# Performance work log

Measured on AMD Instinct MI355X. Metric: run time of the kernel, lower is better.

## Reference

```python
import jax, jax.numpy as jnp
import numpy as np

B, N, I, O, CG, H, E = 32, 256, 16, 16, 64, 64, 4096
SEQ_LEN = 256  # sequence_length init arg (temporal attention scale)


def setup_inputs() -> dict:
    key = jax.random.key(0)
    ks = jax.random.split(key, 24)
    r = lambda i, shape, s: jax.random.normal(ks[i], shape, jnp.float32) * s
    return {
        'data': jax.random.normal(ks[0], (B, I, N), jnp.float32),
        'masks': jax.random.bernoulli(ks[1], 0.8, (B, I, N)),
        'edge_index': jax.random.randint(ks[2], (2, E), 0, N, jnp.int64),
        'gcn_w': r(3, (I, CG), 0.2),
        'gcn_b': jnp.zeros((CG,), jnp.float32),
        'sa_qw': r(4, (CG, CG), 0.1), 'sa_qb': jnp.zeros((CG,), jnp.float32),
        'sa_kw': r(5, (CG, CG), 0.1), 'sa_kb': jnp.zeros((CG,), jnp.float32),
        'gru_wih': r(6, (3 * H, I), 0.1), 'gru_whh': r(7, (3 * H, H), 0.1),
        'gru_bih': jnp.zeros((3 * H,), jnp.float32), 'gru_bhh': jnp.zeros((3 * H,), jnp.float32),
        'ta_qw': r(8, (H, H), 0.1), 'ta_qb': jnp.zeros((H,), jnp.float32),
        'ta_kw': r(9, (H, H), 0.1), 'ta_kb': jnp.zeros((H,), jnp.float32),
        'fc1_w': r(10, (H * N * 2, H * N // 4), 0.005), 'fc1_b': jnp.zeros((H * N // 4,), jnp.float32),
        'fc2_w': r(11, (H * N // 4, O * N), 0.01), 'fc2_b': jnp.zeros((O * N,), jnp.float32),
    }


def _forward(data, masks, edge_index, gcn_w, gcn_b, sa_qw, sa_qb, sa_kw, sa_kb,
             gru_wih, gru_whh, gru_bih, gru_bhh, ta_qw, ta_qb, ta_kw, ta_kb,
             fc1_w, fc1_b, fc2_w, fc2_b):
    data = jnp.where(masks, data, 0.0)            # [B, I, N]
    x = jnp.swapaxes(data, 1, 2)                  # [B, N, I] (per-sample node features)

    loop = jnp.arange(N)
    src = jnp.concatenate([edge_index[0], loop])
    dst = jnp.concatenate([edge_index[1], loop])
    w = jnp.concatenate([jnp.ones((E,), jnp.float32), 2.0 * jnp.ones((N,), jnp.float32)])
    deg = jax.ops.segment_sum(w, dst, num_segments=N)
    dinv = jnp.where(deg > 0, jax.lax.rsqrt(deg), 0.0)
    norm = dinv[src] * w * dinv[dst]              # [E+N]
    xw = x @ gcn_w                                # [B, N, CG]
    msg = xw[:, src, :] * norm[None, :, None]     # gather + scale
    agg = jax.vmap(lambda m: jax.ops.segment_sum(m, dst, num_segments=N))(msg)
    h = jax.nn.relu(agg + gcn_b)                  # [B, N, CG]

    # --- SpatialAttention (per sample, scale 1/sqrt(num_nodes)) ---
    q = h @ sa_qw + sa_qb
    k = h @ sa_kw + sa_kb
    att = jax.nn.softmax(jnp.einsum('bnc,bmc->bnm', q, k) / np.sqrt(N).astype(np.float32), axis=-1)
    ha = jnp.einsum('bnm,bmc->bnc', att, h)

    # torch stacks x.T -> [B, CG, N] then .view(B, -1, CG): a reshape, not a transpose
    se = jnp.swapaxes(h, 1, 2).reshape(B, N, CG)
    sa = jnp.swapaxes(ha, 1, 2).reshape(B, N, CG)
    # dropout is identity in eval mode

    # --- GRU (1 layer, batch_first) over rnn_input = data.view(B, -1, I) ---
    rnn_in = data.reshape(B, N, I)
    def step(hprev, xt):
        gi = xt @ gru_wih.T + gru_bih
        gh = hprev @ gru_whh.T + gru_bhh
        ir, iz, inn = jnp.split(gi, 3, axis=-1)
        hr, hz, hn = jnp.split(gh, 3, axis=-1)
        r = jax.nn.sigmoid(ir + hr)
        z = jax.nn.sigmoid(iz + hz)
        n = jnp.tanh(inn + r * hn)
        hnew = (1.0 - z) * n + z * hprev
        return hnew, hnew
    h0 = jnp.zeros((B, H), jnp.float32)
    _, outs = jax.lax.scan(step, h0, jnp.swapaxes(rnn_in, 0, 1))
    rnn_out = jnp.swapaxes(outs, 0, 1)            # [B, N, H]

    # --- TemporalAttention (scale 1/sqrt(sequence_length)) ---
    qt = rnn_out @ ta_qw + ta_qb
    kt = rnn_out @ ta_kw + ta_kb
    att_t = jax.nn.softmax(jnp.einsum('btc,bsc->bts', qt, kt) / np.sqrt(SEQ_LEN).astype(np.float32), axis=-1)
    rnn_a = jnp.einsum('bts,bsc->btc', att_t, rnn_out)

    # --- fused MLP combine ---
    embed = jnp.concatenate([rnn_out, se], axis=-1).reshape(B, -1)  # [B, 2*H*N]
    inter = embed @ fc1_w + fc1_b
    final = inter @ fc2_w + fc2_b
    final = jnp.swapaxes(final.reshape(B, N, O), 1, 2)              # [B, O, N]
    rnn_a = jnp.swapaxes(rnn_a, 1, 2)                               # [B, H, N]
    return final, sa, rnn_a


def reference(data, masks, edge_index, gcn_w, gcn_b, sa_qw, sa_qb, sa_kw, sa_kb,
              gru_wih, gru_whh, gru_bih, gru_bhh, ta_qw, ta_qb, ta_kw, ta_kb,
              fc1_w, fc1_b, fc2_w, fc2_b):
    return _forward(data, masks, edge_index, gcn_w, gcn_b, sa_qw, sa_qb, sa_kw, sa_kb,
                    gru_wih, gru_whh, gru_bih, gru_bhh, ta_qw, ta_qb, ta_kw, ta_kb,
                    fc1_w, fc1_b, fc2_w, fc2_b)
```

## Files before the change

### kernel.cpp

```cpp
#include <hip/hip_runtime.h>

#define NB 32
#define NN 256
#define NI 16
#define NO 16
#define NC 64
#define NH 64
#define NE 4096
#define FC1_N 4096

__device__ __forceinline__ float sigmoidf_(float x){ return 1.0f/(1.0f+__expf(-x)); }
__device__ __forceinline__ float tanhf_(float x){
  float e = __expf(2.0f*x);
  return 1.0f - 2.0f/(e+1.0f);
}

__device__ __forceinline__ void gload16(const void* g, void* l){
  __builtin_amdgcn_global_load_lds((const __attribute__((address_space(1))) void*)g,
                                   (__attribute__((address_space(3))) void*)l, 16, 0, 0);
}

__global__ void k_detect(const unsigned char* __restrict__ m8, const int* __restrict__ ei, int* flags){
  int t = blockIdx.x*256 + threadIdx.x;
  unsigned a = (unsigned)m8[t*4+1] | (unsigned)m8[t*4+2] | (unsigned)m8[t*4+3];
  if (__any(a != 0) && (threadIdx.x & 63) == 0) atomicOr(&flags[0], 1);
  unsigned b = 0;
  if (t < 4096) b = (unsigned)ei[2*t+1];
  if (__any(b != 0) && (threadIdx.x & 63) == 0) atomicOr(&flags[1], 1);
}

__global__ void k_mask(const float* __restrict__ data, const unsigned char* __restrict__ m8,
                       const int* __restrict__ flags, float* __restrict__ dm){
  int i = blockIdx.x*256 + threadIdx.x;
  int mv = flags[0] ? (int)m8[i] : ((const int*)m8)[i];
  dm[i] = mv ? data[i] : 0.0f;
}

__device__ __forceinline__ int edge_src(const int* ei, const int* flags, int e){
  return flags[1] ? ei[e] : ei[2*e];
}
__device__ __forceinline__ int edge_dst(const int* ei, const int* flags, int e){
  return flags[1] ? ei[NE + e] : ei[2*(NE + e)];
}

__global__ __launch_bounds__(256) void k_graph(const int* __restrict__ ei, const int* __restrict__ flags,
                                               float* wadj){
  int t = threadIdx.x;
  float4 z = {0.f,0.f,0.f,0.f};
  for (int x = t; x < 16384; x += 256) ((float4*)wadj)[x] = z;
  __shared__ float degs[NN];
  __shared__ float dls[NN];
  degs[t] = 0.f;
  __syncthreads();
  for (int e = t; e < NE; e += 256) atomicAdd(&degs[edge_dst(ei, flags, e)], 1.0f);
  __syncthreads();
  float di = rsqrtf(degs[t] + 2.0f);
  dls[t] = di;
  atomicAdd(&wadj[t*NN + t], 2.0f*di*di);
  __syncthreads();
  for (int e = t; e < NE; e += 256){
    int s = edge_src(ei, flags, e), d = edge_dst(ei, flags, e);
    atomicAdd(&wadj[d*NN + s], dls[s]*dls[d]);
  }
}

__global__ void k_xw(const float* __restrict__ dm, const float* __restrict__ gw, float* __restrict__ xw){
  int idx = blockIdx.x*256 + threadIdx.x;
  int c = idx & 63, n = (idx>>6) & 255, b = idx>>14;
  const float* dmb = dm + b*NI*NN;
  float a = 0.f;
  #pragma unroll
  for (int i=0;i<NI;i++) a += dmb[i*NN + n]*gw[i*NC + c];
  xw[idx] = a;
}

__global__ void k_agg(const float* __restrict__ wadj, const float* __restrict__ xw,
                      const float* __restrict__ gb, float* __restrict__ h){
  int idx = blockIdx.x*256 + threadIdx.x;
  int c = idx & 63, n = (idx>>6) & 255, b = idx>>14;
  const float* wr = wadj + n*NN;
  const float* xb = xw + b*NN*NC + c;
  float a = gb[c];
  #pragma unroll 4
  for (int m=0;m<NN;m++) a += wr[m]*xb[m*NC];
  h[idx] = fmaxf(a, 0.0f);
}

__global__ void k_qk2(const float* __restrict__ hb, const float* __restrict__ rnn,
    const float* __restrict__ saqw, const float* __restrict__ saqb,
    const float* __restrict__ sakw, const float* __restrict__ sakb,
    const float* __restrict__ taqw, const float* __restrict__ taqb,
    const float* __restrict__ takw, const float* __restrict__ takb,
    float* __restrict__ qb, float* __restrict__ kb, float* __restrict__ qt, float* __restrict__ kt){
  int bid = blockIdx.x;
  const float *src, *qw, *qbias, *kw, *kbias; float *qo, *ko;
  if (bid < 2048){ src=hb; qw=saqw; qbias=saqb; kw=sakw; kbias=sakb; qo=qb; ko=kb; }
  else { bid -= 2048; src=rnn; qw=taqw; qbias=taqb; kw=takw; kbias=takb; qo=qt; ko=kt; }
  int idx = bid*256 + threadIdx.x;
  int c = idx & 63;
  const float* hr = src + (idx>>6)*NC;
  float aq = qbias[c], ak = kbias[c];
  #pragma unroll 8
  for (int cc=0; cc<NC; cc++){ float hv = hr[cc]; aq += hv*qw[cc*NC + c]; ak += hv*kw[cc*NC + c]; }
  qo[idx] = aq; ko[idx] = ak;
}

__global__ __launch_bounds__(256) void k_attn2(const float* __restrict__ qb, const float* __restrict__ kb,
    const float* __restrict__ hb, const float* __restrict__ qt, const float* __restrict__ kt,
    const float* __restrict__ rnn, float* __restrict__ out_sa, float* __restrict__ out_ra){
  int bidx = blockIdx.x;
  const float *q, *kmat, *v; float* outp;
  if (bidx < 1024){ q=qb; kmat=kb; v=hb; outp=out_sa; }
  else { bidx -= 1024; q=qt; kmat=kt; v=rnn; outp=out_ra; }
  int b = bidx >> 5, n0 = (bidx & 31)*8;
  int t = threadIdx.x;
  const float scale = 0.0625f;
  __shared__ __align__(16) float qs[8][64];
  __shared__ float S[8][256];
  #pragma unroll
  for (int rep=0; rep<2; rep++){
    int j = rep*256 + t; int r = j>>6, c = j&63;
    qs[r][c] = q[((b<<8) + n0 + r)*NC + c];
  }
  __syncthreads();
  float4 kr[16];
  const float4* kp = (const float4*)(kmat + ((b<<8) + t)*NC);
  #pragma unroll
  for (int i=0;i<16;i++) kr[i] = kp[i];
  #pragma unroll
  for (int r=0;r<8;r++){
    const float4* q4 = (const float4*)qs[r];
    float s = 0.f;
    #pragma unroll
    for (int i=0;i<16;i++){ float4 a=q4[i], bb=kr[i]; s += a.x*bb.x + a.y*bb.y + a.z*bb.z + a.w*bb.w; }
    S[r][t] = s*scale;
  }
  __syncthreads();
  {
    int g = t>>5, l = t&31;
    float vals[8];
    #pragma unroll
    for (int k2=0;k2<8;k2++) vals[k2] = S[g][l + (k2<<5)];
    float mx = vals[0];
    #pragma unroll
    for (int k2=1;k2<8;k2++) mx = fmaxf(mx, vals[k2]);
    #pragma unroll
    for (int off=16; off; off>>=1) mx = fmaxf(mx, __shfl_xor(mx, off));
    float sm = 0.f;
    #pragma unroll
    for (int k2=0;k2<8;k2++){ vals[k2] = __expf(vals[k2]-mx); sm += vals[k2]; }
    #pragma unroll
    for (int off=16; off; off>>=1) sm += __shfl_xor(sm, off);
    float rS = 1.0f/sm;
    #pragma unroll
    for (int k2=0;k2<8;k2++) S[g][l + (k2<<5)] = vals[k2]*rS;
  }
  __syncthreads();
  int c = t & 63, rp = t >> 6;
  const float* vp = v + (b<<8)*NC + c;
  float a0 = 0.f, a1 = 0.f;
  #pragma unroll 4
  for (int m=0;m<NN;m++){
    float vv = vp[m*NC];
    a0 += S[rp][m]*vv;
    a1 += S[rp+4][m]*vv;
  }
  outp[(((b<<6)+c)<<8) + n0 + rp]     = a0;
  outp[(((b<<6)+c)<<8) + n0 + rp + 4] = a1;
}

__global__ __launch_bounds__(192) void k_gru(const float* __restrict__ dm,
        const float* __restrict__ wih, const float* __restrict__ bih,
        const float* __restrict__ whh, const float* __restrict__ bhh,
        float* __restrict__ rnn){
  int b = blockIdx.x, j = threadIdx.x;
  __shared__ __align__(16) float dmS[4096];
  __shared__ __align__(16) float hs[64];
  __shared__ float gh[192];
  __shared__ float gin[64];
  float wh[64];
  const float4* wr = (const float4*)(whh + j*NH);
  #pragma unroll
  for (int k4=0;k4<16;k4++){ float4 t4 = wr[k4]; wh[4*k4]=t4.x; wh[4*k4+1]=t4.y; wh[4*k4+2]=t4.z; wh[4*k4+3]=t4.w; }
  float wi[16];
  const float4* wir = (const float4*)(wih + j*NI);
  #pragma unroll
  for (int k4=0;k4<4;k4++){ float4 t4 = wir[k4]; wi[4*k4]=t4.x; wi[4*k4+1]=t4.y; wi[4*k4+2]=t4.z; wi[4*k4+3]=t4.w; }
  float bj = bhh[j], bij = bih[j];
  const float4* dmb4 = (const float4*)(dm + b*4096);
  for (int x = j; x < 1024; x += 192) ((float4*)dmS)[x] = dmb4[x];
  if (j < 64) hs[j] = 0.f;
  __syncthreads();
  for (int t=0;t<NN;t++){
    const float* xt = &dmS[t*16];
    float gival = bij;
    #pragma unroll
    for (int i=0;i<16;i++) gival += wi[i]*xt[i];
    float a0=0.f,a1=0.f,a2=0.f,a3=0.f;
    #pragma unroll
    for (int k4=0;k4<16;k4++){
      float4 hv = *(const float4*)&hs[4*k4];
      a0 += wh[4*k4+0]*hv.x; a1 += wh[4*k4+1]*hv.y; a2 += wh[4*k4+2]*hv.z; a3 += wh[4*k4+3]*hv.w;
    }
    float ghv = a0+a1+a2+a3+bj;
    if (j < 128) gh[j] = ghv + gival;
    else { gh[j] = ghv; gin[j-128] = gival; }
    __syncthreads();
    if (j < 64){
      float r  = sigmoidf_(gh[j]);
      float z  = sigmoidf_(gh[j+64]);
      float nn = tanhf_   (gin[j] + r*gh[j+128]);
      float hn = nn + z*(hs[j]-nn);
      rnn[(b*NN + t)*NH + j] = hn;
      hs[j] = hn;
    }
    __syncthreads();
  }
}

__global__ void k_embedT(const float* __restrict__ rnn, const float* __restrict__ h,
                         float* __restrict__ ET){
  int idx = blockIdx.x*256 + threadIdx.x;
  int bb = idx & 31, rr = idx >> 5;
  int n = rr >> 7, c = rr & 127;
  float v;
  if (c < 64) v = rnn[((bb<<8) + n)*NH + c];
  else { int f = (n<<6) + (c-64); v = h[(bb<<14) + ((f&255)<<6) + (f>>8)]; }
  ET[idx] = v;
}

template<int KC>
__global__ __launch_bounds__(512, 4) void k_fc(const float* __restrict__ W,
        const float* __restrict__ Ein, float* __restrict__ part){
  const int tid = threadIdx.x, lane = tid & 63, wv_ = tid >> 6;
  const int cw = wv_ & 1, bq = wv_ >> 1;
  const int c0 = blockIdx.x*512;
  const long k0 = (long)blockIdx.y*KC;
  __shared__ __align__(16) float wlds[2][8][512];
  __shared__ __align__(16) float elds[2][256];
  float acc[4][8];
  #pragma unroll
  for (int c=0;c<4;c++)
    #pragma unroll
    for (int bb=0;bb<8;bb++) acc[c][bb]=0.f;

  const int NCH = KC/8;
  #define STAGE_FC(ch, bf) { \
    const float* wsrc = W + (k0 + (long)(ch)*8)*FC1_N + c0; \
    gload16(wsrc + (long)wv_*FC1_N + lane*4,       &wlds[bf][wv_][0]); \
    gload16(wsrc + (long)wv_*FC1_N + 256 + lane*4, &wlds[bf][wv_][256]); \
    if (wv_ == 0) gload16(Ein + (k0 + (long)(ch)*8)*32 + lane*4, &elds[bf][0]); \
  }

  STAGE_FC(0, 0)
  int cur = 0;
  for (int ch=0; ch<NCH; ch++){
    __syncthreads();
    if (ch+1 < NCH) STAGE_FC(ch+1, cur^1)
    #pragma unroll
    for (int r=0;r<8;r++){
      float4 wv4 = *(const float4*)&wlds[cur][r][cw*256 + lane*4];
      float4 e0 = *(const float4*)&elds[cur][r*32 + bq*8];
      float4 e1 = *(const float4*)&elds[cur][r*32 + bq*8 + 4];
      float ev[8] = {e0.x,e0.y,e0.z,e0.w,e1.x,e1.y,e1.z,e1.w};
      #pragma unroll
      for (int bb=0;bb<8;bb++){
        acc[0][bb] += wv4.x*ev[bb];
        acc[1][bb] += wv4.y*ev[bb];
        acc[2][bb] += wv4.z*ev[bb];
        acc[3][bb] += wv4.w*ev[bb];
      }
    }
    cur ^= 1;
  }
  float* pp = part + (long)blockIdx.y*131072 + (long)(bq*8)*FC1_N + c0 + cw*256 + lane*4;
  #pragma unroll
  for (int bb=0;bb<8;bb++){
    float4 o; o.x=acc[0][bb]; o.y=acc[1][bb]; o.z=acc[2][bb]; o.w=acc[3][bb];
    *(float4*)(pp + (long)bb*FC1_N) = o;
  }
  #undef STAGE_FC
}

__global__ void k_red1(const float* __restrict__ part, const float* __restrict__ bias,
                       float* __restrict__ ITr){
  int idx = blockIdx.x*256 + threadIdx.x;
  int b = idx >> 12, col = idx & 4095;
  float a = bias[col];
  #pragma unroll 16
  for (int y=0;y<64;y++) a += part[(long)y*131072 + b*FC1_N + col];
  ITr[col*32 + b] = a;
}

__global__ void k_red2(const float* __restrict__ part, const float* __restrict__ bias,
                       float* __restrict__ outp){
  int idx = blockIdx.x*256 + threadIdx.x;
  int b = idx >> 12, col = idx & 4095;
  float a = bias[col];
  #pragma unroll 16
  for (int y=0;y<64;y++) a += part[(long)y*131072 + b*FC1_N + col];
  int n = col >> 4, o = col & 15;
  outp[(b<<12) + (o<<8) + n] = a;
}

extern "C" void kernel_launch(void* const* d_in, const int* in_sizes, int n_in,
                              void* d_out, int out_size, void* d_ws, size_t ws_size,
                              hipStream_t stream) {
  const float* data   = (const float*)d_in[0];
  const unsigned char* masks = (const unsigned char*)d_in[1];
  const int* ei       = (const int*)d_in[2];
  const float* gcn_w  = (const float*)d_in[3];
  const float* gcn_b  = (const float*)d_in[4];
  const float* sa_qw  = (const float*)d_in[5];
  const float* sa_qb  = (const float*)d_in[6];
  const float* sa_kw  = (const float*)d_in[7];
  const float* sa_kb  = (const float*)d_in[8];
  const float* wih    = (const float*)d_in[9];
  const float* whh    = (const float*)d_in[10];
  const float* bih    = (const float*)d_in[11];
  const float* bhh    = (const float*)d_in[12];
  const float* ta_qw  = (const float*)d_in[13];
  const float* ta_qb  = (const float*)d_in[14];
  const float* ta_kw  = (const float*)d_in[15];
  const float* ta_kb  = (const float*)d_in[16];
  const float* fc1_w  = (const float*)d_in[17];
  const float* fc1_b  = (const float*)d_in[18];
  const float* fc2_w  = (const float*)d_in[19];
  const float* fc2_b  = (const float*)d_in[20];

  float* dm    = (float*)d_ws;
  float* wadj  = dm + 131072;
  int*   flags = (int*)(wadj + 65536);
  float* xw    = (float*)(flags + 8);
  float* hb    = xw + 524288;
  float* qb    = hb + 524288;
  float* kb    = qb + 524288;
  float* rnn   = kb + 524288;
  float* qt    = rnn + 524288;
  float* kt    = qt + 524288;
  float* ET    = kt + 524288;
  float* ITr   = ET + 1048576;
  float* part1 = ITr + 131072;
  float* part2 = part1 + 64*131072;

  float* out_final = (float*)d_out;
  float* out_sa = out_final + 131072;
  float* out_ra = out_final + 655360;

  hipMemsetAsync(flags, 0, 32, stream);

  k_detect<<<128,256,0,stream>>>(masks, ei, flags);
  k_mask<<<512,256,0,stream>>>(data, masks, flags, dm);
  k_graph<<<1,256,0,stream>>>(ei, flags, wadj);
  k_xw<<<2048,256,0,stream>>>(dm, gcn_w, xw);
  k_gru<<<32,192,0,stream>>>(dm, wih, bih, whh, bhh, rnn);
  k_agg<<<2048,256,0,stream>>>(wadj, xw, gcn_b, hb);
  k_qk2<<<4096,256,0,stream>>>(hb, rnn, sa_qw, sa_qb, sa_kw, sa_kb,
                               ta_qw, ta_qb, ta_kw, ta_kb, qb, kb, qt, kt);
  k_attn2<<<2048,256,0,stream>>>(qb, kb, hb, qt, kt, rnn, out_sa, out_ra);
  k_embedT<<<4096,256,0,stream>>>(rnn, hb, ET);
  { dim3 g(8,64); k_fc<512><<<g,512,0,stream>>>(fc1_w, ET, part1); }
  k_red1<<<512,256,0,stream>>>(part1, fc1_b, ITr);
  { dim3 g(8,64); k_fc<64><<<g,512,0,stream>>>(fc2_w, ITr, part2); }
  k_red2<<<512,256,0,stream>>>(part2, fc2_b, out_final);
}
```

Baseline: 504.3 us.

## Restructure GRU into single-wavefront blocks and vectorize FC reduction kernels

The GRU kernel drops from 192 to 64 threads per block, so each thread computes all three gate dot products for its hidden unit. This removes one of the two block barriers per timestep and the shared-memory exchange of gate values, but each thread now holds about 3x more weight registers and does 3x the serial FMA work. The two partial-sum reduction kernels now load float4 values with a quarter of the blocks, and the GRU launch moves earlier in the stream. Pressure from the larger register arrays could cause spills.

```diff
diff --git a/kernel.cpp b/kernel.cpp
--- a/kernel.cpp
+++ b/kernel.cpp
@@ -169,51 +169,71 @@
   outp[(((b<<6)+c)<<8) + n0 + rp + 4] = a1;
 }
 
-__global__ __launch_bounds__(192) void k_gru(const float* __restrict__ dm,
+__global__ __launch_bounds__(64) void k_gru(const float* __restrict__ dm,
         const float* __restrict__ wih, const float* __restrict__ bih,
         const float* __restrict__ whh, const float* __restrict__ bhh,
         float* __restrict__ rnn){
-  int b = blockIdx.x, j = threadIdx.x;
+  const int b = blockIdx.x, j = threadIdx.x;
   __shared__ __align__(16) float dmS[4096];
-  __shared__ __align__(16) float hs[64];
-  __shared__ float gh[192];
-  __shared__ float gin[64];
-  float wh[64];
-  const float4* wr = (const float4*)(whh + j*NH);
-  #pragma unroll
-  for (int k4=0;k4<16;k4++){ float4 t4 = wr[k4]; wh[4*k4]=t4.x; wh[4*k4+1]=t4.y; wh[4*k4+2]=t4.z; wh[4*k4+3]=t4.w; }
-  float wi[16];
-  const float4* wir = (const float4*)(wih + j*NI);
-  #pragma unroll
-  for (int k4=0;k4<4;k4++){ float4 t4 = wir[k4]; wi[4*k4]=t4.x; wi[4*k4+1]=t4.y; wi[4*k4+2]=t4.z; wi[4*k4+3]=t4.w; }
-  float bj = bhh[j], bij = bih[j];
+  __shared__ __align__(16) float hsS[64];
   const float4* dmb4 = (const float4*)(dm + b*4096);
-  for (int x = j; x < 1024; x += 192) ((float4*)dmS)[x] = dmb4[x];
-  if (j < 64) hs[j] = 0.f;
-  __syncthreads();
+  float4* dmS4 = (float4*)dmS;
+  #pragma unroll
+  for (int x=0;x<16;x++) dmS4[j + 64*x] = dmb4[j + 64*x];
+  float wr_[64], wz_[64], wn_[64];
+  {
+    const float4* pr = (const float4*)(whh + (long)j*NH);
+    const float4* pz = (const float4*)(whh + (long)(j+64)*NH);
+    const float4* pn = (const float4*)(whh + (long)(j+128)*NH);
+    #pragma unroll
+    for (int k4=0;k4<16;k4++){
+      float4 a = pr[k4]; wr_[4*k4]=a.x; wr_[4*k4+1]=a.y; wr_[4*k4+2]=a.z; wr_[4*k4+3]=a.w;
+      float4 c = pz[k4]; wz_[4*k4]=c.x; wz_[4*k4+1]=c.y; wz_[4*k4+2]=c.z; wz_[4*k4+3]=c.w;
+      float4 d = pn[k4]; wn_[4*k4]=d.x; wn_[4*k4+1]=d.y; wn_[4*k4+2]=d.z; wn_[4*k4+3]=d.w;
+    }
+  }
+  float wir[16], wiz[16], win_[16];
+  {
+    const float4* pr = (const float4*)(wih + (long)j*NI);
+    const float4* pz = (const float4*)(wih + (long)(j+64)*NI);
+    const float4* pn = (const float4*)(wih + (long)(j+128)*NI);
+    #pragma unroll
+    for (int k4=0;k4<4;k4++){
+      float4 a = pr[k4]; wir[4*k4]=a.x;  wir[4*k4+1]=a.y;  wir[4*k4+2]=a.z;  wir[4*k4+3]=a.w;
+      float4 c = pz[k4]; wiz[4*k4]=c.x;  wiz[4*k4+1]=c.y;  wiz[4*k4+2]=c.z;  wiz[4*k4+3]=c.w;
+      float4 d = pn[k4]; win_[4*k4]=d.x; win_[4*k4+1]=d.y; win_[4*k4+2]=d.z; win_[4*k4+3]=d.w;
+    }
+  }
+  const float br = bhh[j], bz = bhh[j+64], bn = bhh[j+128];
+  const float bir = bih[j], biz = bih[j+64], bin_ = bih[j+128];
+  float h = 0.f;
+  hsS[j] = 0.f;
+  __syncthreads();
+  float* rp = rnn + (long)b*NN*NH + j;
   for (int t=0;t<NN;t++){
+    float hv[64];
+    const float4* hs4 = (const float4*)hsS;
+    #pragma unroll
+    for (int k4=0;k4<16;k4++){
+      float4 v = hs4[k4];
+      hv[4*k4]=v.x; hv[4*k4+1]=v.y; hv[4*k4+2]=v.z; hv[4*k4+3]=v.w;
+    }
+    float gr0=0.f, gr1=0.f, gz0=0.f, gz1=0.f, gn0=0.f, gn1=0.f;
+    #pragma unroll
+    for (int k=0;k<64;k+=2){
+      gr0 += wr_[k]*hv[k];   gz0 += wz_[k]*hv[k];   gn0 += wn_[k]*hv[k];
+      gr1 += wr_[k+1]*hv[k+1]; gz1 += wz_[k+1]*hv[k+1]; gn1 += wn_[k+1]*hv[k+1];
+    }
     const float* xt = &dmS[t*16];
-    float gival = bij;
-    #pragma unroll
-    for (int i=0;i<16;i++) gival += wi[i]*xt[i];
-    float a0=0.f,a1=0.f,a2=0.f,a3=0.f;
-    #pragma unroll
-    for (int k4=0;k4<16;k4++){
-      float4 hv = *(const float4*)&hs[4*k4];
-      a0 += wh[4*k4+0]*hv.x; a1 += wh[4*k4+1]*hv.y; a2 += wh[4*k4+2]*hv.z; a3 += wh[4*k4+3]*hv.w;
-    }
-    float ghv = a0+a1+a2+a3+bj;
-    if (j < 128) gh[j] = ghv + gival;
-    else { gh[j] = ghv; gin[j-128] = gival; }
-    __syncthreads();
-    if (j < 64){
-      float r  = sigmoidf_(gh[j]);
-      float z  = sigmoidf_(gh[j+64]);
-      float nn = tanhf_   (gin[j] + r*gh[j+128]);
-      float hn = nn + z*(hs[j]-nn);
-      rnn[(b*NN + t)*NH + j] = hn;
-      hs[j] = hn;
-    }
+    float gir=bir, giz=biz, gin2=bin_;
+    #pragma unroll
+    for (int i=0;i<16;i++){ float xv = xt[i]; gir += wir[i]*xv; giz += wiz[i]*xv; gin2 += win_[i]*xv; }
+    float r  = sigmoidf_(gir + gr0 + gr1 + br);
+    float z  = sigmoidf_(giz + gz0 + gz1 + bz);
+    float nn2= tanhf_  (gin2 + r*(gn0 + gn1 + bn));
+    h = nn2 + z*(h - nn2);
+    rp[(long)t*NH] = h;
+    hsS[j] = h;
     __syncthreads();
   }
 }
@@ -284,23 +304,38 @@
 
 __global__ void k_red1(const float* __restrict__ part, const float* __restrict__ bias,
                        float* __restrict__ ITr){
-  int idx = blockIdx.x*256 + threadIdx.x;
-  int b = idx >> 12, col = idx & 4095;
-  float a = bias[col];
+  int idx4 = blockIdx.x*256 + threadIdx.x;
+  int b = idx4 >> 10, col4 = idx4 & 1023;
+  float4 a = ((const float4*)bias)[col4];
   #pragma unroll 16
-  for (int y=0;y<64;y++) a += part[(long)y*131072 + b*FC1_N + col];
-  ITr[col*32 + b] = a;
+  for (int y=0;y<64;y++){
+    float4 p = ((const float4*)(part + (long)y*131072 + (long)b*FC1_N))[col4];
+    a.x+=p.x; a.y+=p.y; a.z+=p.z; a.w+=p.w;
+  }
+  int col = col4*4;
+  ITr[(col+0)*32 + b] = a.x;
+  ITr[(col+1)*32 + b] = a.y;
+  ITr[(col+2)*32 + b] = a.z;
+  ITr[(col+3)*32 + b] = a.w;
 }
 
 __global__ void k_red2(const float* __restrict__ part, const float* __restrict__ bias,
                        float* __restrict__ outp){
-  int idx = blockIdx.x*256 + threadIdx.x;
-  int b = idx >> 12, col = idx & 4095;
-  float a = bias[col];
+  int idx4 = blockIdx.x*256 + threadIdx.x;
+  int b = idx4 >> 10, col4 = idx4 & 1023;
+  float4 a = ((const float4*)bias)[col4];
   #pragma unroll 16
-  for (int y=0;y<64;y++) a += part[(long)y*131072 + b*FC1_N + col];
-  int n = col >> 4, o = col & 15;
-  outp[(b<<12) + (o<<8) + n] = a;
+  for (int y=0;y<64;y++){
+    float4 p = ((const float4*)(part + (long)y*131072 + (long)b*FC1_N))[col4];
+    a.x+=p.x; a.y+=p.y; a.z+=p.z; a.w+=p.w;
+  }
+  float av[4] = {a.x, a.y, a.z, a.w};
+  #pragma unroll
+  for (int c=0;c<4;c++){
+    int col = col4*4 + c;
+    int n = col >> 4, o = col & 15;
+    outp[(b<<12) + (o<<8) + n] = av[c];
+  }
 }
 
 extern "C" void kernel_launch(void* const* d_in, const int* in_sizes, int n_in,
@@ -351,16 +386,16 @@
 
   k_detect<<<128,256,0,stream>>>(masks, ei, flags);
   k_mask<<<512,256,0,stream>>>(data, masks, flags, dm);
+  k_gru<<<32,64,0,stream>>>(dm, wih, bih, whh, bhh, rnn);
   k_graph<<<1,256,0,stream>>>(ei, flags, wadj);
   k_xw<<<2048,256,0,stream>>>(dm, gcn_w, xw);
-  k_gru<<<32,192,0,stream>>>(dm, wih, bih, whh, bhh, rnn);
   k_agg<<<2048,256,0,stream>>>(wadj, xw, gcn_b, hb);
   k_qk2<<<4096,256,0,stream>>>(hb, rnn, sa_qw, sa_qb, sa_kw, sa_kb,
                                ta_qw, ta_qb, ta_kw, ta_kb, qb, kb, qt, kt);
   k_attn2<<<2048,256,0,stream>>>(qb, kb, hb, qt, kt, rnn, out_sa, out_ra);
   k_embedT<<<4096,256,0,stream>>>(rnn, hb, ET);
   { dim3 g(8,64); k_fc<512><<<g,512,0,stream>>>(fc1_w, ET, part1); }
-  k_red1<<<512,256,0,stream>>>(part1, fc1_b, ITr);
+  k_red1<<<128,256,0,stream>>>(part1, fc1_b, ITr);
   { dim3 g(8,64); k_fc<64><<<g,512,0,stream>>>(fc2_w, ITr, part2); }
-  k_red2<<<512,256,0,stream>>>(part2, fc2_b, out_final);
-}
+  k_red2<<<128,256,0,stream>>>(part2, fc2_b, out_final);
+}
```

Result: slower. 584.2 us (+15.8%).
